# Performance work log

Measured on AMD Instinct MI355X. Metric: run time of the kernel, lower is better.

Reference implementation:

```python
import jax, jax.numpy as jnp
import numpy as np

K = 8
WRM = 40


def _gru(x, h, w_ih, w_hh, b_ih, b_hh):
    # PyTorch GRU cell: gates ordered (r, z, n)
    gi = x @ w_ih.T + b_ih
    gh = h @ w_hh.T + b_hh
    i_r, i_z, i_n = jnp.split(gi, 3, axis=-1)
    h_r, h_z, h_n = jnp.split(gh, 3, axis=-1)
    r = jax.nn.sigmoid(i_r + h_r)
    z = jax.nn.sigmoid(i_z + h_z)
    n = jnp.tanh(i_n + r * h_n)
    return (1.0 - z) * n + z * h


def setup_inputs() -> dict:
    key = jax.random.key(0)
    ks = jax.random.split(key, 20)
    T, B, C, Wd, H = 240, 64, 1, 84, 84
    N, M, E, A = 512, 256, 32, 18
    D = C * Wd * H
    u = lambda k, s, sc: jax.random.uniform(k, s, jnp.float32, -sc, sc)
    sM = float(1.0 / np.sqrt(M))
    sD = float(1.0 / np.sqrt(D))
    return dict(
        obs_seq=jax.random.normal(ks[0], (T, B, C, Wd, H), jnp.float32),
        act_seq=jax.random.randint(ks[1], (T, B), 0, A),
        w_enc=u(ks[2], (N, D), sD), b_enc=u(ks[3], (N,), sD),
        w_ih=u(ks[4], (3 * M, N), sM), w_hh=u(ks[5], (3 * M, M), sM),
        b_ih=u(ks[6], (3 * M,), sM), b_hh=u(ks[7], (3 * M,), sM),
        w_ih_c=u(ks[8], (3 * M, E), sM), w_hh_c=u(ks[9], (3 * M, M), sM),
        b_ih_c=u(ks[10], (3 * M,), sM), b_hh_c=u(ks[11], (3 * M,), sM),
        W1=u(ks[12], (M, M), sM), b1=u(ks[13], (M,), sM),
        W2=u(ks[14], (N, M), sM), b2=u(ks[15], (N,), sM),
        emb=jax.random.normal(ks[16], (A, E), jnp.float32),
    )


def reference(obs_seq, act_seq, w_enc, b_enc, w_ih, w_hh, b_ih, b_hh,
              w_ih_c, w_hh_c, b_ih_c, b_hh_c, W1, b1, W2, b2, emb):
    T, B = obs_seq.shape[0], obs_seq.shape[1]
    M = w_hh.shape[1]
    # encoder: flatten + linear -> (T, B, N)
    z = obs_seq.reshape(T, B, -1) @ w_enc.T + b_enc
    wrm_seq, trn_seq = z[:WRM], z[WRM:]
    acts = act_seq[WRM:]

    h0 = jnp.zeros((B, M), z.dtype)
    warm_hn, _ = jax.lax.scan(
        lambda h, x: (_gru(x, h, w_ih, w_hh, b_ih, b_hh), None), h0, wrm_seq)
    warm_hn = jax.lax.stop_gradient(warm_hn)  # torch.no_grad() warmup

    def cls_step(h, x):
        h2 = _gru(x, h, w_ih, w_hh, b_ih, b_hh)
        return h2, h2

    _, bts = jax.lax.scan(cls_step, warm_hn, trn_seq)  # (T', B, M)

    Tp = bts.shape[0]
    Tout = Tp - K
    idx = jnp.arange(Tout)[:, None] + jnp.arange(K)[None, :]  # (Tout, K)
    act_win = emb[acts[idx]]  # (Tout, K, B, E)

    def open_step(h, x):  # h: (Tout, B, M), x: (Tout, B, E)
        h2 = _gru(x, h, w_ih_c, w_hh_c, b_ih_c, b_hh_c)
        zt = jax.nn.relu(h2 @ W1.T + b1) @ W2.T + b2
        return h2, zt

    _, zs = jax.lax.scan(open_step, bts[:Tout], jnp.transpose(act_win, (1, 0, 2, 3)))
    return jnp.transpose(zs, (1, 0, 2, 3))  # (Tout, K, B, N)
```

## Files before the change

### kernel.cpp

```cpp
#include <hip/hip_runtime.h>
#include <hip/hip_fp16.h>
#include <math.h>

#define TT   240
#define BBATCH 64
#define DDIM 7056
#define KENC_PAD 7072
#define NENC 512
#define MHID 256
#define G3   768
#define WRMC 40
#define KWIN 8
#define TOUTC 192
#define RROWS (TOUTC*BBATCH)
#define NSTEPS (WRMC + TOUTC)

#define B_GI     ((size_t)0)
#define B_WENCH  ((size_t)0)
#define B_GBH    ((size_t)0)
#define B_R1H    ((size_t)37748736)
#define B_ZH     ((size_t)45613056)
#define B_HOPEN  ((size_t)45613056)
#define B_BTS    ((size_t)60817408)
#define B_BTSH   ((size_t)73400320)
#define B_HOPENH ((size_t)79691776)
#define B_WIHH   ((size_t)85983232)
#define B_WHHCH  ((size_t)86769664)
#define B_W1H    ((size_t)87162880)
#define B_W2H    ((size_t)87293952)
#define B_GTAB   ((size_t)87556096)
#define B_WT8    ((size_t)87611392)

typedef _Float16 half8 __attribute__((ext_vector_type(8)));
typedef _Float16 h2v  __attribute__((ext_vector_type(2)));
typedef __attribute__((ext_vector_type(4))) float f32x4;

__device__ __forceinline__ float sigmf(float x) { return 1.0f / (1.0f + expf(-x)); }
__device__ __forceinline__ h2v u2h2(unsigned int u) {
  union { unsigned int u; h2v h; } c; c.u = u; return c.h;
}

__global__ void wconv_kernel(const float* __restrict__ W, __half* __restrict__ o,
                             int N, int K, int Kpad) {
  const int idx = blockIdx.x * 256 + threadIdx.x;
  if (idx >= N * Kpad) return;
  const int n = idx / Kpad, k = idx % Kpad;
  o[idx] = __float2half((k < K) ? W[(size_t)n * K + k] : 0.f);
}

template<int AF32>
__global__ __launch_bounds__(256, 3) void gemm_hp(
    const void* __restrict__ A, const __half* __restrict__ W,
    const float* __restrict__ bias, void* __restrict__ C,
    int M, int N, int K, int Kpad, int relu, int out_h, int outk)
{
  __shared__ __half Ah[2][64][40];
  __shared__ __half Bh[2][256][40];
  const int tid = threadIdx.x;
  const int bx = blockIdx.x, by = blockIdx.y;
  const int w = tid >> 6;
  const int lane = tid & 63;
  const int l15 = lane & 15;
  const int khalf = (lane >> 4) * 8;
  const int arow = tid >> 2;
  const int akq = (tid & 3) * 8;
  const int bn = tid >> 2, bk = (tid & 3) * 8;

  f32x4 acc[4][4];
#pragma unroll
  for (int i = 0; i < 4; ++i)
#pragma unroll
    for (int j = 0; j < 4; ++j) acc[i][j] = (f32x4){0.f, 0.f, 0.f, 0.f};

  const int niter = Kpad / 32;

  float4 raA0, raA1, rahA, rbA0, rbA1, rbA2, rbA3;
  float4 raB0, raB1, rahB, rbB0, rbB1, rbB2, rbB3;

#define LOADT(IT, ra0, ra1, rah, rb0, rb1, rb2, rb3)                              \
  {                                                                               \
    const int k0_ = (IT) * 32;                                                    \
    if (AF32) {                                                                   \
      const float* Af_ = (const float*)A;                                         \
      ra0 = make_float4(0.f, 0.f, 0.f, 0.f); ra1 = ra0;                           \
      const size_t base_ = (size_t)(by * 64 + arow) * K + k0_ + akq;              \
      if (k0_ + akq < K)     ra0 = *(const float4*)(Af_ + base_);                 \
      if (k0_ + akq + 4 < K) ra1 = *(const float4*)(Af_ + base_ + 4);             \
    } else {                                                                      \
      rah = *(const float4*)((const __half*)A +                                   \
            (size_t)(by * 64 + arow) * Kpad + k0_ + akq);                         \
    }                                                                             \
    rb0 = *(const float4*)(W + (size_t)(bx * 256 + bn      ) * Kpad + k0_ + bk);  \
    rb1 = *(const float4*)(W + (size_t)(bx * 256 + bn +  64) * Kpad + k0_ + bk);  \
    rb2 = *(const float4*)(W + (size_t)(bx * 256 + bn + 128) * Kpad + k0_ + bk);  \
    rb3 = *(const float4*)(W + (size_t)(bx * 256 + bn + 192) * Kpad + k0_ + bk);  \
  }

#define BODY(IT, ra0, ra1, rah, rb0, rb1, rb2, rb3)                               \
  {                                                                               \
    __half (*Ac)[40] = Ah[(IT) & 1];                                              \
    __half (*Bc)[40] = Bh[(IT) & 1];                                              \
    if (AF32) {                                                                   \
      __half2 hh_[4];                                                             \
      hh_[0] = __floats2half2_rn(ra0.x, ra0.y);                                   \
      hh_[1] = __floats2half2_rn(ra0.z, ra0.w);                                   \
      hh_[2] = __floats2half2_rn(ra1.x, ra1.y);                                   \
      hh_[3] = __floats2half2_rn(ra1.z, ra1.w);                                   \
      *(float4*)&Ac[arow][akq] = *(float4*)hh_;                                   \
    } else {                                                                      \
      *(float4*)&Ac[arow][akq] = rah;                                             \
    }                                                                             \
    *(float4*)&Bc[bn      ][bk] = rb0;                                            \
    *(float4*)&Bc[bn +  64][bk] = rb1;                                            \
    *(float4*)&Bc[bn + 128][bk] = rb2;                                            \
    *(float4*)&Bc[bn + 192][bk] = rb3;                                            \
    __syncthreads();                                                              \
    if ((IT) + 2 < niter)                                                         \
      LOADT((IT) + 2, ra0, ra1, rah, rb0, rb1, rb2, rb3);                         \
    half8 ah_[4], bh_[4];                                                         \
    _Pragma("unroll")                                                             \
    for (int i = 0; i < 4; ++i) ah_[i] = *(half8*)&Ac[i * 16 + l15][khalf];       \
    _Pragma("unroll")                                                             \
    for (int j = 0; j < 4; ++j) bh_[j] = *(half8*)&Bc[w * 64 + j * 16 + l15][khalf]; \
    _Pragma("unroll")                                                             \
    for (int i = 0; i < 4; ++i)                                                   \
      _Pragma("unroll")                                                           \
      for (int j = 0; j < 4; ++j)                                                 \
        acc[i][j] = __builtin_amdgcn_mfma_f32_16x16x32_f16(ah_[i], bh_[j], acc[i][j], 0, 0, 0); \
  }

  LOADT(0, raA0, raA1, rahA, rbA0, rbA1, rbA2, rbA3);
  if (niter > 1) LOADT(1, raB0, raB1, rahB, rbB0, rbB1, rbB2, rbB3);

  int it = 0;
  while (true) {
    BODY(it, raA0, raA1, rahA, rbA0, rbA1, rbA2, rbA3);
    ++it; if (it == niter) break;
    BODY(it, raB0, raB1, rahB, rbB0, rbB1, rbB2, rbB3);
    ++it; if (it == niter) break;
  }
#undef BODY
#undef LOADT

  const int r4 = (lane >> 4) * 4;
#pragma unroll
  for (int j = 0; j < 4; ++j) {
    const int col = bx * 256 + w * 64 + j * 16 + l15;
    const float bc = bias ? bias[col] : 0.f;
#pragma unroll
    for (int i = 0; i < 4; ++i) {
      const int mbase = by * 64 + i * 16 + r4;
#pragma unroll
      for (int r = 0; r < 4; ++r) {
        const int m = mbase + r;
        float vv = acc[i][j][r] + bc;
        if (relu) vv = fmaxf(vv, 0.f);
        if (outk >= 0) {
          const int t = m >> 6, b = m & 63;
          ((float*)C)[(((size_t)(t * KWIN + outk) * BBATCH + b) * NENC) + col] = vv;
        } else if (out_h) {
          ((__half*)C)[(size_t)m * N + col] = __float2half(vv);
        } else {
          ((float*)C)[(size_t)m * N + col] = vv;
        }
      }
    }
  }
}

__global__ void gitab_kernel(const float* __restrict__ emb, const float* __restrict__ w_ih_c,
                             const float* __restrict__ b_ih_c, float* __restrict__ gt)
{
  const int idx = blockIdx.x * blockDim.x + threadIdx.x;
  if (idx >= 18 * G3) return;
  const int a = idx / G3, cgate = idx % G3;
  float s = b_ih_c[cgate];
#pragma unroll
  for (int e = 0; e < 32; ++e) s = fmaf(emb[a * 32 + e], w_ih_c[cgate * 32 + e], s);
  gt[idx] = s;
}

__global__ void transpose_whh_p8(const float* __restrict__ w, float4* __restrict__ wt8) {
  const int id = blockIdx.x * 256 + threadIdx.x;
  if (id >= 32 * G3) return;
  const int k8 = id / G3, j = id % G3;
  const float* src = w + (size_t)j * MHID + k8 * 8;
  __half2 h2[4];
#pragma unroll
  for (int q = 0; q < 4; ++q)
    h2[q] = __floats2half2_rn(src[2 * q], src[2 * q + 1]);
  wt8[id] = *(float4*)h2;
}

__global__ __launch_bounds__(768, 3) void scan4_kernel(
    const float* __restrict__ gi_all, const float4* __restrict__ wt8,
    const float* __restrict__ b_hh, float* __restrict__ bts,
    __half* __restrict__ bts_h)
{
  const int b = blockIdx.x;
  const int j = threadIdx.x;
  __shared__ __align__(16) float hs[256];
  __shared__ __align__(16) __half hs16[256];
  __shared__ float gacc[768];

  unsigned int wreg[128];
#pragma unroll
  for (int k8 = 0; k8 < 32; ++k8) {
    const float4 v = wt8[(size_t)k8 * G3 + j];
    const uint4 u = *(const uint4*)&v;
    wreg[k8 * 4 + 0] = u.x; wreg[k8 * 4 + 1] = u.y;
    wreg[k8 * 4 + 2] = u.z; wreg[k8 * 4 + 3] = u.w;
  }
  const float bj = b_hh[j];
  if (j < 256) { hs[j] = 0.f; hs16[j] = __float2half(0.f); }
  __syncthreads();

  const uint4* h16v = (const uint4*)hs16;

  for (int t = 0; t < NSTEPS; ++t) {
    float gr = 0.f, gz = 0.f, gn = 0.f;
    if (j < 256) {
      const float* gp = gi_all + ((size_t)t * BBATCH + b) * G3;
      gr = gp[j]; gz = gp[256 + j]; gn = gp[512 + j];
    }

    float a0 = bj, a1 = 0.f, a2 = 0.f, a3 = 0.f;
#pragma unroll
    for (int k8 = 0; k8 < 32; ++k8) {
      const uint4 hu = h16v[k8];
#if __has_builtin(__builtin_amdgcn_fdot2)
      a0 = __builtin_amdgcn_fdot2(u2h2(wreg[k8 * 4 + 0]), u2h2(hu.x), a0, false);
      a1 = __builtin_amdgcn_fdot2(u2h2(wreg[k8 * 4 + 1]), u2h2(hu.y), a1, false);
      a2 = __builtin_amdgcn_fdot2(u2h2(wreg[k8 * 4 + 2]), u2h2(hu.z), a2, false);
      a3 = __builtin_amdgcn_fdot2(u2h2(wreg[k8 * 4 + 3]), u2h2(hu.w), a3, false);
#else
      {
        const h2v w0 = u2h2(wreg[k8 * 4 + 0]), w1 = u2h2(wreg[k8 * 4 + 1]);
        const h2v w2 = u2h2(wreg[k8 * 4 + 2]), w3 = u2h2(wreg[k8 * 4 + 3]);
        const h2v x0 = u2h2(hu.x), x1 = u2h2(hu.y), x2 = u2h2(hu.z), x3 = u2h2(hu.w);
        a0 = fmaf((float)w0.x, (float)x0.x, a0); a0 = fmaf((float)w0.y, (float)x0.y, a0);
        a1 = fmaf((float)w1.x, (float)x1.x, a1); a1 = fmaf((float)w1.y, (float)x1.y, a1);
        a2 = fmaf((float)w2.x, (float)x2.x, a2); a2 = fmaf((float)w2.y, (float)x2.y, a2);
        a3 = fmaf((float)w3.x, (float)x3.x, a3); a3 = fmaf((float)w3.y, (float)x3.y, a3);
      }
#endif
    }
    gacc[j] = (a0 + a1) + (a2 + a3);
    __syncthreads();

    if (j < 256) {
      const float r = sigmf(gr + gacc[j]);
      const float z = sigmf(gz + gacc[256 + j]);
      const float n = tanhf(gn + r * gacc[512 + j]);
      const float hn = (1.f - z) * n + z * hs[j];
      hs[j] = hn;
      hs16[j] = __float2half(hn);
      if (t >= WRMC) {
        const size_t o = (((size_t)(t - WRMC)) * BBATCH + b) * MHID + j;
        bts[o] = hn;
        bts_h[o] = __float2half(hn);
      }
    }
    __syncthreads();
  }
}

__global__ __launch_bounds__(256) void open_gates(
    const float* __restrict__ gtab, const int* __restrict__ act_seq,
    const __half* __restrict__ gh, const float* __restrict__ hin,
    float* __restrict__ hout, __half* __restrict__ hout_h, int kstep)
{
  const int row = blockIdx.x;
  const int j = threadIdx.x;
  const int t = row >> 6, b = row & 63;
  const int a = act_seq[(WRMC + t + kstep) * BBATCH + b];
  const float* gi = gtab + a * G3;
  const float gr = gi[j], gz = gi[256 + j], gn = gi[512 + j];
  const size_t g0 = (size_t)row * G3;
  const float hr = __half2float(gh[g0 + j]);
  const float hz = __half2float(gh[g0 + 256 + j]);
  const float hnn = __half2float(gh[g0 + 512 + j]);
  const float h = hin[(size_t)row * MHID + j];
  const float r = sigmf(gr + hr);
  const float z = sigmf(gz + hz);
  const float n = tanhf(gn + r * hnn);
  const float hn = (1.f - z) * n + z * h;
  hout[(size_t)row * MHID + j] = hn;
  hout_h[(size_t)row * MHID + j] = __float2half(hn);
}

extern "C" void kernel_launch(void* const* d_in, const int* in_sizes, int n_in,
                              void* d_out, int out_size, void* d_ws, size_t ws_size,
                              hipStream_t stream) {
  const float* obs    = (const float*)d_in[0];
  const int*   act    = (const int*)  d_in[1];
  const float* w_enc  = (const float*)d_in[2];
  const float* b_enc  = (const float*)d_in[3];
  const float* w_ih   = (const float*)d_in[4];
  const float* w_hh   = (const float*)d_in[5];
  const float* b_ih   = (const float*)d_in[6];
  const float* b_hh   = (const float*)d_in[7];
  const float* w_ih_c = (const float*)d_in[8];
  const float* w_hh_c = (const float*)d_in[9];
  const float* b_ih_c = (const float*)d_in[10];
  const float* b_hh_c = (const float*)d_in[11];
  const float* W1     = (const float*)d_in[12];
  const float* b1     = (const float*)d_in[13];
  const float* W2     = (const float*)d_in[14];
  const float* b2     = (const float*)d_in[15];
  const float* emb    = (const float*)d_in[16];

  char* wsb = (char*)d_ws;
  float* out = (float*)d_out;

  float*  gi      = (float*)(wsb + B_GI);
  __half* gbh     = (__half*)(wsb + B_GBH);
  __half* r1_h    = (__half*)(wsb + B_R1H);
  __half* z_h     = (__half*)(wsb + B_ZH);
  float*  hopen   = (float*)(wsb + B_HOPEN);
  float*  bts     = (float*)(wsb + B_BTS);
  __half* bts_h   = (__half*)(wsb + B_BTSH);
  __half* hopen_h = (__half*)(wsb + B_HOPENH);
  __half* enc_h   = (__half*)(wsb + B_WENCH);
  __half* ih_h    = (__half*)(wsb + B_WIHH);
  __half* hhc_h   = (__half*)(wsb + B_WHHCH);
  __half* w1_h    = (__half*)(wsb + B_W1H);
  __half* w2_h    = (__half*)(wsb + B_W2H);
  float*  gtab    = (float*)(wsb + B_GTAB);
  float4* wt8     = (float4*)(wsb + B_WT8);

  const dim3 blk(256);

  wconv_kernel<<<(NENC * KENC_PAD + 255) / 256, blk, 0, stream>>>(w_enc, enc_h, NENC, DDIM, KENC_PAD);
  wconv_kernel<<<(G3 * NENC + 255) / 256, blk, 0, stream>>>(w_ih, ih_h, G3, NENC, NENC);
  wconv_kernel<<<(G3 * MHID + 255) / 256, blk, 0, stream>>>(w_hh_c, hhc_h, G3, MHID, MHID);
  wconv_kernel<<<(MHID * MHID + 255) / 256, blk, 0, stream>>>(W1, w1_h, MHID, MHID, MHID);
  wconv_kernel<<<(NENC * MHID + 255) / 256, blk, 0, stream>>>(W2, w2_h, NENC, MHID, MHID);
  gitab_kernel<<<54, 256, 0, stream>>>(emb, w_ih_c, b_ih_c, gtab);
  transpose_whh_p8<<<(32 * G3 + 255) / 256, blk, 0, stream>>>(w_hh, wt8);

  gemm_hp<1><<<dim3(NENC / 256, NSTEPS * BBATCH / 64), blk, 0, stream>>>(
      obs, enc_h, b_enc, z_h, NSTEPS * BBATCH, NENC, DDIM, KENC_PAD, 0, 1, -1);
  gemm_hp<0><<<dim3(G3 / 256, NSTEPS * BBATCH / 64), blk, 0, stream>>>(
      z_h, ih_h, b_ih, gi, NSTEPS * BBATCH, G3, NENC, NENC, 0, 0, -1);

  scan4_kernel<<<BBATCH, 768, 0, stream>>>(gi, wt8, b_hh, bts, bts_h);

  for (int k = 0; k < KWIN; ++k) {
    const __half* hin_h = (k == 0) ? bts_h : hopen_h;
    const float*  hin   = (k == 0) ? bts   : hopen;
    gemm_hp<0><<<dim3(G3 / 256, RROWS / 64), blk, 0, stream>>>(
        hin_h, hhc_h, b_hh_c, gbh, RROWS, G3, MHID, MHID, 0, 1, -1);
    open_gates<<<RROWS, 256, 0, stream>>>(gtab, act, gbh, hin, hopen, hopen_h, k);
    gemm_hp<0><<<dim3(MHID / 256, RROWS / 64), blk, 0, stream>>>(
        hopen_h, w1_h, b1, r1_h, RROWS, MHID, MHID, MHID, 1, 1, -1);
    gemm_hp<0><<<dim3(NENC / 256, RROWS / 64), blk, 0, stream>>>(
        r1_h, w2_h, b2, out, RROWS, NENC, MHID, MHID, 0, 0, k);
  }
}
```

Measured before the change: 1.090 ms.

## Split-K the encoder GEMM into two halves with a separate reduce kernel

The large encoder GEMM (14848x512, K=7056) used to launch only 2x232 blocks. It now splits K into two halves across blockIdx.z, doubling the block count to improve occupancy across the CUs. Each half writes fp32 partials to a new workspace region, and a reduce kernel sums them, adds the bias and converts to fp16. The K padding grows so each half is a multiple of 32. In exchange, the partials add extra global traffic of about 2x30MB written and read, plus one more kernel launch.

```diff
diff --git a/kernel.cpp b/kernel.cpp
--- a/kernel.cpp
+++ b/kernel.cpp
@@ -5,7 +5,7 @@
 #define TT   240
 #define BBATCH 64
 #define DDIM 7056
-#define KENC_PAD 7072
+#define KENC_PAD 7104
 #define NENC 512
 #define MHID 256
 #define G3   768
@@ -14,14 +14,16 @@
 #define TOUTC 192
 #define RROWS (TOUTC*BBATCH)
 #define NSTEPS (WRMC + TOUTC)
+#define MN_Z ((size_t)14848*512)
 
 #define B_GI     ((size_t)0)
 #define B_WENCH  ((size_t)0)
 #define B_GBH    ((size_t)0)
+#define B_P      ((size_t)8388608)
 #define B_R1H    ((size_t)37748736)
-#define B_ZH     ((size_t)45613056)
 #define B_HOPEN  ((size_t)45613056)
 #define B_BTS    ((size_t)60817408)
+#define B_ZH     ((size_t)69206016)
 #define B_BTSH   ((size_t)73400320)
 #define B_HOPENH ((size_t)79691776)
 #define B_WIHH   ((size_t)85983232)
@@ -46,6 +48,116 @@
   if (idx >= N * Kpad) return;
   const int n = idx / Kpad, k = idx % Kpad;
   o[idx] = __float2half((k < K) ? W[(size_t)n * K + k] : 0.f);
+}
+
+__global__ __launch_bounds__(256, 3) void gemm_enc_sk(
+    const float* __restrict__ A, const __half* __restrict__ W,
+    float* __restrict__ P, int M, int N, int K, int Kpad)
+{
+  __shared__ __half Ah[2][64][40];
+  __shared__ __half Bh[2][256][40];
+  const int tid = threadIdx.x;
+  const int bx = blockIdx.x, by = blockIdx.y, bz = blockIdx.z;
+  const int w = tid >> 6;
+  const int lane = tid & 63;
+  const int l15 = lane & 15;
+  const int khalf = (lane >> 4) * 8;
+  const int arow = tid >> 2;
+  const int akq = (tid & 3) * 8;
+  const int bn = tid >> 2, bk = (tid & 3) * 8;
+  const int kbeg = bz * (Kpad / 2);
+  const int niter = (Kpad / 2) / 32;
+
+  f32x4 acc[4][4];
+#pragma unroll
+  for (int i = 0; i < 4; ++i)
+#pragma unroll
+    for (int j = 0; j < 4; ++j) acc[i][j] = (f32x4){0.f, 0.f, 0.f, 0.f};
+
+  float4 raA0, raA1, rbA0, rbA1, rbA2, rbA3;
+  float4 raB0, raB1, rbB0, rbB1, rbB2, rbB3;
+
+#define LOADT(IT, ra0, ra1, rb0, rb1, rb2, rb3)                                   \
+  {                                                                               \
+    const int k0_ = kbeg + (IT) * 32;                                             \
+    ra0 = make_float4(0.f, 0.f, 0.f, 0.f); ra1 = ra0;                             \
+    const size_t base_ = (size_t)(by * 64 + arow) * K + k0_ + akq;                \
+    if (k0_ + akq < K)     ra0 = *(const float4*)(A + base_);                     \
+    if (k0_ + akq + 4 < K) ra1 = *(const float4*)(A + base_ + 4);                 \
+    rb0 = *(const float4*)(W + (size_t)(bx * 256 + bn      ) * Kpad + k0_ + bk);  \
+    rb1 = *(const float4*)(W + (size_t)(bx * 256 + bn +  64) * Kpad + k0_ + bk);  \
+    rb2 = *(const float4*)(W + (size_t)(bx * 256 + bn + 128) * Kpad + k0_ + bk);  \
+    rb3 = *(const float4*)(W + (size_t)(bx * 256 + bn + 192) * Kpad + k0_ + bk);  \
+  }
+
+#define BODY(IT, ra0, ra1, rb0, rb1, rb2, rb3)                                    \
+  {                                                                               \
+    __half (*Ac)[40] = Ah[(IT) & 1];                                              \
+    __half (*Bc)[40] = Bh[(IT) & 1];                                              \
+    __half2 hh_[4];                                                               \
+    hh_[0] = __floats2half2_rn(ra0.x, ra0.y);                                     \
+    hh_[1] = __floats2half2_rn(ra0.z, ra0.w);                                     \
+    hh_[2] = __floats2half2_rn(ra1.x, ra1.y);                                     \
+    hh_[3] = __floats2half2_rn(ra1.z, ra1.w);                                     \
+    *(float4*)&Ac[arow][akq] = *(float4*)hh_;                                     \
+    *(float4*)&Bc[bn      ][bk] = rb0;                                            \
+    *(float4*)&Bc[bn +  64][bk] = rb1;                                            \
+    *(float4*)&Bc[bn + 128][bk] = rb2;                                            \
+    *(float4*)&Bc[bn + 192][bk] = rb3;                                            \
+    __syncthreads();                                                              \
+    if ((IT) + 2 < niter)                                                         \
+      LOADT((IT) + 2, ra0, ra1, rb0, rb1, rb2, rb3);                              \
+    half8 ah_[4], bh_[4];                                                         \
+    _Pragma("unroll")                                                             \
+    for (int i = 0; i < 4; ++i) ah_[i] = *(half8*)&Ac[i * 16 + l15][khalf];       \
+    _Pragma("unroll")                                                             \
+    for (int j = 0; j < 4; ++j) bh_[j] = *(half8*)&Bc[w * 64 + j * 16 + l15][khalf]; \
+    _Pragma("unroll")                                                             \
+    for (int i = 0; i < 4; ++i)                                                   \
+      _Pragma("unroll")                                                           \
+      for (int j = 0; j < 4; ++j)                                                 \
+        acc[i][j] = __builtin_amdgcn_mfma_f32_16x16x32_f16(ah_[i], bh_[j], acc[i][j], 0, 0, 0); \
+  }
+
+  LOADT(0, raA0, raA1, rbA0, rbA1, rbA2, rbA3);
+  LOADT(1, raB0, raB1, rbB0, rbB1, rbB2, rbB3);
+
+  int it = 0;
+  while (true) {
+    BODY(it, raA0, raA1, rbA0, rbA1, rbA2, rbA3);
+    ++it; if (it == niter) break;
+    BODY(it, raB0, raB1, rbB0, rbB1, rbB2, rbB3);
+    ++it; if (it == niter) break;
+  }
+#undef BODY
+#undef LOADT
+
+  float* Pb = P + (size_t)bz * MN_Z;
+  const int r4 = (lane >> 4) * 4;
+#pragma unroll
+  for (int j = 0; j < 4; ++j) {
+    const int col = bx * 256 + w * 64 + j * 16 + l15;
+#pragma unroll
+    for (int i = 0; i < 4; ++i) {
+      const int mbase = by * 64 + i * 16 + r4;
+#pragma unroll
+      for (int r = 0; r < 4; ++r)
+        Pb[(size_t)(mbase + r) * N + col] = acc[i][j][r];
+    }
+  }
+}
+
+__global__ void zreduce_kernel(const float* __restrict__ P, const float* __restrict__ bias,
+                               __half* __restrict__ z) {
+  const size_t i4 = ((size_t)blockIdx.x * 256 + threadIdx.x) * 4;
+  if (i4 >= MN_Z) return;
+  const float4 a = *(const float4*)(P + i4);
+  const float4 b = *(const float4*)(P + MN_Z + i4);
+  const int col = (int)(i4 & 511);
+  __half2 h0 = __floats2half2_rn(a.x + b.x + bias[col],     a.y + b.y + bias[col + 1]);
+  __half2 h1 = __floats2half2_rn(a.z + b.z + bias[col + 2], a.w + b.w + bias[col + 3]);
+  __half2 hh[2] = {h0, h1};
+  *(float2*)(z + i4) = *(float2*)hh;
 }
 
 template<int AF32>
@@ -315,6 +427,7 @@
 
   float*  gi      = (float*)(wsb + B_GI);
   __half* gbh     = (__half*)(wsb + B_GBH);
+  float*  P       = (float*)(wsb + B_P);
   __half* r1_h    = (__half*)(wsb + B_R1H);
   __half* z_h     = (__half*)(wsb + B_ZH);
   float*  hopen   = (float*)(wsb + B_HOPEN);
@@ -339,8 +452,10 @@
   gitab_kernel<<<54, 256, 0, stream>>>(emb, w_ih_c, b_ih_c, gtab);
   transpose_whh_p8<<<(32 * G3 + 255) / 256, blk, 0, stream>>>(w_hh, wt8);
 
-  gemm_hp<1><<<dim3(NENC / 256, NSTEPS * BBATCH / 64), blk, 0, stream>>>(
-      obs, enc_h, b_enc, z_h, NSTEPS * BBATCH, NENC, DDIM, KENC_PAD, 0, 1, -1);
+  gemm_enc_sk<<<dim3(NENC / 256, NSTEPS * BBATCH / 64, 2), blk, 0, stream>>>(
+      obs, enc_h, P, NSTEPS * BBATCH, NENC, DDIM, KENC_PAD);
+  zreduce_kernel<<<(int)((MN_Z / 4 + 255) / 256), blk, 0, stream>>>(P, b_enc, z_h);
+
   gemm_hp<0><<<dim3(G3 / 256, NSTEPS * BBATCH / 64), blk, 0, stream>>>(
       z_h, ih_h, b_ih, gi, NSTEPS * BBATCH, G3, NENC, NENC, 0, 0, -1);
 
```

Result: slower. 1.853 ms (+70.1%).
